# Performance work log

Hardware: AMD Instinct MI355X
Metric: run time of the kernel (lower is better)

The kernel has to match this reference:

```python
import jax, jax.numpy as jnp
import numpy as np

BLOCK = 8
C = 64


def setup_inputs() -> dict:
    key = jax.random.key(0)
    k = jax.random.split(key, 6)
    B, H, W = 4, 512, 512
    x = jax.random.normal(k[0], (B, C, H, W), jnp.float32)
    # per-channel 8x8 transform matrices (torch.randn init)
    tw = jax.random.normal(k[1], (C, BLOCK, BLOCK), jnp.float32)
    s = 1.0 / np.sqrt(C).astype(np.float32)
    w1 = jax.random.normal(k[2], (C, C), jnp.float32) * s  # 1x1 conv weight [out,in]
    b1 = jax.random.normal(k[3], (C,), jnp.float32) * s
    w2 = jax.random.normal(k[4], (C, C), jnp.float32) * s
    b2 = jax.random.normal(k[5], (C,), jnp.float32) * s
    return {"x": x, "tw": tw, "w1": w1, "b1": b1, "w2": w2, "b2": b2}


def reference(x, tw, w1, b1, w2, b2):
    B, Cc, H, W = x.shape
    bs = BLOCK
    nh, nw = H // bs, W // bs
    # extract 8x8 blocks: [b,c,nh,nw,i,j]
    p = x.reshape(B, Cc, nh, bs, nw, bs).transpose(0, 1, 2, 4, 3, 5)
    # per-channel T @ P @ T^T : out[p,q] = T[p,i] P[i,j] T[q,j]
    t = jnp.einsum('cpi,bcnmij,cqj->bcnmpq', tw, p, tw)
    # fold blocks back to image
    y = t.transpose(0, 1, 2, 4, 3, 5).reshape(B, Cc, H, W)
    # quantization gate: 1x1 conv -> relu -> 1x1 conv -> sigmoid
    g = jnp.einsum('oc,bchw->bohw', w1, y) + b1[None, :, None, None]
    g = jax.nn.relu(g)
    g = jnp.einsum('oc,bchw->bohw', w2, g) + b2[None, :, None, None]
    g = jax.nn.sigmoid(g)
    return y * g
```

## Files before the change

kernel.cpp:

```cpp
#include <hip/hip_runtime.h>

typedef float f4 __attribute__((ext_vector_type(4)));
typedef __attribute__((ext_vector_type(4))) float f32x4;
typedef _Float16 h8 __attribute__((ext_vector_type(8)));

__device__ __forceinline__ void gload_lds16(const float* g, float* l) {
    __builtin_amdgcn_global_load_lds(
        (const __attribute__((address_space(1))) void*)g,
        (__attribute__((address_space(3))) void*)l, 16, 0, 0);
}

__global__ __launch_bounds__(256, 2)
void avif_pipe(const float* __restrict__ x, const float* __restrict__ twm,
               const float* __restrict__ w1, const float* __restrict__ b1,
               const float* __restrict__ w2, const float* __restrict__ b2,
               float* __restrict__ out)
{
    __shared__ float xs[8192];
    __shared__ ushort ysf[128][64];
    __shared__ ushort hsf[128][64];

    const int t = threadIdx.x;
    const int bid = blockIdx.x;
    const int wc = bid & 1;
    const int hb = (bid >> 1) & 63;
    const int b  = bid >> 7;

    const int wv = t >> 6, lane = t & 63;
    const int li = lane & 15, lg = lane >> 4, l7 = li & 7;
    const int lb3 = (li >> 3) << 2;

    const float* xslab = x + (((size_t)(b * 64)) * 512 + (size_t)hb * 8) * 512 + wc * 256;
    const float* gp[8];
#pragma unroll
    for (int j = 0; j < 8; ++j) {
        const int G = j * 256 + t;
        const int c = G >> 5;
        const int v = (G & 31) ^ (c & 7);
        const int r = v >> 2, qg = v & 3;
        gp[j] = xslab + (size_t)c * 262144 + r * 512 + qg * 4;
    }
    float* lbase = &xs[wv * 256];

    h8 w1f[2], w2f[2];
    {
        const float* p1 = w1 + (16 * wv + li) * 64 + lg * 8;
        const float* p2 = w2 + (16 * wv + li) * 64 + lg * 8;
#pragma unroll
        for (int kk = 0; kk < 2; ++kk) {
            f4 a = *(const f4*)(p1 + kk * 32);
            f4 d = *(const f4*)(p1 + kk * 32 + 4);
            h8 f;
#pragma unroll
            for (int q = 0; q < 4; ++q) { f[q] = (_Float16)a[q]; f[4 + q] = (_Float16)d[q]; }
            w1f[kk] = f;
            a = *(const f4*)(p2 + kk * 32);
            d = *(const f4*)(p2 + kk * 32 + 4);
#pragma unroll
            for (int q = 0; q < 4; ++q) { f[q] = (_Float16)a[q]; f[4 + q] = (_Float16)d[q]; }
            w2f[kk] = f;
        }
    }
    const int o0 = 16 * wv + 4 * lg;
    const f4 b1v = *(const f4*)(b1 + o0);
    const float b2s = b2[16 * wv + li];
    const int sg0 = ((lg       ^ l7 ^ lb3) << 3);
    const int sg1 = (((4 + lg) ^ l7 ^ lb3) << 3);
    const int go  = o0 >> 3, co = 4 * (lg & 1);
    const int ch  = 16 * wv + li;
    const int cgE = ch >> 3, c7E = li & 7;

    const int pid = t >> 1, h2 = t & 1;
    const int c   = pid & 63, blk = pid >> 6, Q0 = 4 * h2;
    const float* tB = twm + c * 64;
    const int sc = c * 128, swc = c & 7;
    const int cg = c >> 3, c7 = c & 7;

#pragma unroll
    for (int j = 0; j < 8; ++j) gload_lds16(gp[j], lbase + j * 1024);
    asm volatile("s_waitcnt vmcnt(0)" ::: "memory");
    __syncthreads();

    for (int tile = 0; tile < 16; ++tile) {
        const int wt = wc * 16 + tile;

        {
            float M[8][4];
            {
                f4 Ph[8];
#pragma unroll
                for (int i = 0; i < 8; ++i)
                    Ph[i] = *(const f4*)&xs[sc + ((i * 4 + blk * 2) ^ swc) * 4];
#pragma unroll
                for (int qq = 0; qq < 4; ++qq) {
                    f4 Th = *(const f4*)(tB + (Q0 + qq) * 8);
#pragma unroll
                    for (int i = 0; i < 8; ++i) {
                        float s = Ph[i][0] * Th[0];
                        s = fmaf(Ph[i][1], Th[1], s);
                        s = fmaf(Ph[i][2], Th[2], s);
                        s = fmaf(Ph[i][3], Th[3], s);
                        M[i][qq] = s;
                    }
                }
#pragma unroll
                for (int i = 0; i < 8; ++i)
                    Ph[i] = *(const f4*)&xs[sc + ((i * 4 + blk * 2 + 1) ^ swc) * 4];
#pragma unroll
                for (int qq = 0; qq < 4; ++qq) {
                    f4 Th = *(const f4*)(tB + (Q0 + qq) * 8 + 4);
#pragma unroll
                    for (int i = 0; i < 8; ++i) {
                        float s = M[i][qq];
                        s = fmaf(Ph[i][0], Th[0], s);
                        s = fmaf(Ph[i][1], Th[1], s);
                        s = fmaf(Ph[i][2], Th[2], s);
                        s = fmaf(Ph[i][3], Th[3], s);
                        M[i][qq] = s;
                    }
                }
            }
#pragma unroll
            for (int p = 0; p < 8; ++p) {
                f4 a = *(const f4*)(tB + p * 8);
                f4 d = *(const f4*)(tB + p * 8 + 4);
                const int px0 = p * 16 + blk * 8;
#pragma unroll
                for (int qq = 0; qq < 4; ++qq) {
                    const int q = Q0 + qq;
                    float s = a[0] * M[0][qq];
                    s = fmaf(a[1], M[1][qq], s);
                    s = fmaf(a[2], M[2][qq], s);
                    s = fmaf(a[3], M[3][qq], s);
                    s = fmaf(d[0], M[4][qq], s);
                    s = fmaf(d[1], M[5][qq], s);
                    s = fmaf(d[2], M[6][qq], s);
                    s = fmaf(d[3], M[7][qq], s);
                    const int idx = ((cg ^ q ^ (blk << 2)) << 3) | c7;
                    *(_Float16*)&ysf[px0 + q][idx] = (_Float16)s;
                }
            }
        }
        __syncthreads();

        if (tile < 15) {
#pragma unroll
            for (int j = 0; j < 8; ++j)
                gload_lds16(gp[j] + (tile + 1) * 16, lbase + j * 1024);
        }

        f32x4 acc[8];
#pragma unroll
        for (int j = 0; j < 8; ++j) acc[j] = (f32x4){0.f, 0.f, 0.f, 0.f};
#pragma unroll
        for (int j = 0; j < 8; ++j) {
            const int row = 16 * j + li;
            h8 bh0 = *(const h8*)&ysf[row][sg0];
            h8 bh1 = *(const h8*)&ysf[row][sg1];
            acc[j] = __builtin_amdgcn_mfma_f32_16x16x32_f16(w1f[0], bh0, acc[j], 0, 0, 0);
            acc[j] = __builtin_amdgcn_mfma_f32_16x16x32_f16(w1f[1], bh1, acc[j], 0, 0, 0);
        }
#pragma unroll
        for (int j = 0; j < 8; ++j) {
            const int px = 16 * j + li;
            const int idx = ((go ^ l7 ^ lb3) << 3) + co;
            union { _Float16 h[2]; unsigned u; } p01, p23;
            p01.h[0] = (_Float16)fmaxf(acc[j][0] + b1v[0], 0.f);
            p01.h[1] = (_Float16)fmaxf(acc[j][1] + b1v[1], 0.f);
            p23.h[0] = (_Float16)fmaxf(acc[j][2] + b1v[2], 0.f);
            p23.h[1] = (_Float16)fmaxf(acc[j][3] + b1v[3], 0.f);
            *(unsigned*)&hsf[px][idx]     = p01.u;
            *(unsigned*)&hsf[px][idx + 2] = p23.u;
        }
        asm volatile("s_waitcnt vmcnt(0)" ::: "memory");
        __syncthreads();

#pragma unroll
        for (int j = 0; j < 8; ++j) acc[j] = (f32x4){0.f, 0.f, 0.f, 0.f};
#pragma unroll
        for (int j = 0; j < 8; ++j) {
            const int row = 16 * j + li;
            h8 ah0 = *(const h8*)&hsf[row][sg0];
            h8 ah1 = *(const h8*)&hsf[row][sg1];
            acc[j] = __builtin_amdgcn_mfma_f32_16x16x32_f16(ah0, w2f[0], acc[j], 0, 0, 0);
            acc[j] = __builtin_amdgcn_mfma_f32_16x16x32_f16(ah1, w2f[1], acc[j], 0, 0, 0);
        }
        float* oB = out + ((size_t)(b * 64) + ch) * 262144
                    + (size_t)(hb * 8) * 512 + wt * 16 + 4 * lg;
#pragma unroll
        for (int j = 0; j < 8; ++j) {
            f4 r;
#pragma unroll
            for (int r4 = 0; r4 < 4; ++r4) {
                const int pc = 4 * lg + r4;
                const int px = 16 * j + pc;
                const int idx = ((cgE ^ (pc & 7) ^ (((pc >> 3) & 1) << 2)) << 3) | c7E;
                float yv = (float)(*(const _Float16*)&ysf[px][idx]);
                float z = acc[j][r4] + b2s;
                float g = __builtin_amdgcn_rcpf(1.f + __expf(-z));
                r[r4] = yv * g;
            }
            *(f4*)(oB + (size_t)j * 512) = r;
        }
        __syncthreads();
    }
}

extern "C" void kernel_launch(void* const* d_in, const int* in_sizes, int n_in,
                              void* d_out, int out_size, void* d_ws, size_t ws_size,
                              hipStream_t stream) {
    (void)in_sizes; (void)n_in; (void)out_size; (void)d_ws; (void)ws_size;
    const float* x   = (const float*)d_in[0];
    const float* twm = (const float*)d_in[1];
    const float* w1  = (const float*)d_in[2];
    const float* b1  = (const float*)d_in[3];
    const float* w2  = (const float*)d_in[4];
    const float* b2  = (const float*)d_in[5];
    float* out = (float*)d_out;

    avif_pipe<<<dim3(512), dim3(256), 0, stream>>>(x, twm, w1, b1, w2, b2, out);
}
```

Before: 170.2 us.

## Load input blocks directly into registers and split work across more blocks

Drops the LDS staging buffer for the input slab. Each thread now loads its own 8x4 half-block straight into registers and exchanges the other half with its pair via a lane shuffle, prefetching the next tile's registers during compute. The grid grows from 512 to 2048 blocks, each doing 4 interleaved tiles instead of 16, and occupancy is raised to 3 blocks per SM. Barriers become a raw s_barrier with only an lgkmcnt wait. This frees LDS and raises parallelism, at the cost of uncoalesced 16-byte global loads and more register pressure.

```diff
diff --git a/kernel.cpp b/kernel.cpp
--- a/kernel.cpp
+++ b/kernel.cpp
@@ -4,43 +4,29 @@
 typedef __attribute__((ext_vector_type(4))) float f32x4;
 typedef _Float16 h8 __attribute__((ext_vector_type(8)));
 
-__device__ __forceinline__ void gload_lds16(const float* g, float* l) {
-    __builtin_amdgcn_global_load_lds(
-        (const __attribute__((address_space(1))) void*)g,
-        (__attribute__((address_space(3))) void*)l, 16, 0, 0);
-}
-
-__global__ __launch_bounds__(256, 2)
-void avif_pipe(const float* __restrict__ x, const float* __restrict__ twm,
-               const float* __restrict__ w1, const float* __restrict__ b1,
-               const float* __restrict__ w2, const float* __restrict__ b2,
-               float* __restrict__ out)
+#define BAR() do { asm volatile("s_waitcnt lgkmcnt(0)" ::: "memory"); \
+    __builtin_amdgcn_s_barrier(); asm volatile("" ::: "memory"); } while (0)
+
+__global__ __launch_bounds__(256, 3)
+void avif_reg(const float* __restrict__ x, const float* __restrict__ twm,
+              const float* __restrict__ w1, const float* __restrict__ b1,
+              const float* __restrict__ w2, const float* __restrict__ b2,
+              float* __restrict__ out)
 {
-    __shared__ float xs[8192];
     __shared__ ushort ysf[128][64];
     __shared__ ushort hsf[128][64];
 
     const int t = threadIdx.x;
     const int bid = blockIdx.x;
-    const int wc = bid & 1;
-    const int hb = (bid >> 1) & 63;
-    const int b  = bid >> 7;
+    const int wc = (bid >> 3) & 1;
+    const int u  = ((bid >> 4) << 3) | (bid & 7);
+    const int ks = u & 3;
+    const int hb = (u >> 2) & 63;
+    const int b  = u >> 8;
 
     const int wv = t >> 6, lane = t & 63;
     const int li = lane & 15, lg = lane >> 4, l7 = li & 7;
     const int lb3 = (li >> 3) << 2;
-
-    const float* xslab = x + (((size_t)(b * 64)) * 512 + (size_t)hb * 8) * 512 + wc * 256;
-    const float* gp[8];
-#pragma unroll
-    for (int j = 0; j < 8; ++j) {
-        const int G = j * 256 + t;
-        const int c = G >> 5;
-        const int v = (G & 31) ^ (c & 7);
-        const int r = v >> 2, qg = v & 3;
-        gp[j] = xslab + (size_t)c * 262144 + r * 512 + qg * 4;
-    }
-    float* lbase = &xs[wv * 256];
 
     h8 w1f[2], w2f[2];
     {
@@ -73,81 +59,73 @@
     const int pid = t >> 1, h2 = t & 1;
     const int c   = pid & 63, blk = pid >> 6, Q0 = 4 * h2;
     const float* tB = twm + c * 64;
-    const int sc = c * 128, swc = c & 7;
+    const float* xb = x + ((size_t)(b * 64 + c) * 512 + hb * 8) * 512
+                        + blk * 8 + 4 * h2;
     const int cg = c >> 3, c7 = c & 7;
 
-#pragma unroll
-    for (int j = 0; j < 8; ++j) gload_lds16(gp[j], lbase + j * 1024);
-    asm volatile("s_waitcnt vmcnt(0)" ::: "memory");
-    __syncthreads();
-
-    for (int tile = 0; tile < 16; ++tile) {
-        const int wt = wc * 16 + tile;
-
+    int wt = 2 * (ks * 4) + wc;
+
+    f4 Pr[8];
+#pragma unroll
+    for (int i = 0; i < 8; ++i)
+        Pr[i] = *(const f4*)(xb + (size_t)i * 512 + wt * 16);
+
+#pragma unroll 1
+    for (int it = 0; it < 4; ++it) {
+        float M[8][4];
         {
-            float M[8][4];
-            {
-                f4 Ph[8];
-#pragma unroll
-                for (int i = 0; i < 8; ++i)
-                    Ph[i] = *(const f4*)&xs[sc + ((i * 4 + blk * 2) ^ swc) * 4];
+            f4 Tq0[4], Tq1[4];
+#pragma unroll
+            for (int qq = 0; qq < 4; ++qq) {
+                Tq0[qq] = *(const f4*)(tB + (Q0 + qq) * 8 + 4 * h2);
+                Tq1[qq] = *(const f4*)(tB + (Q0 + qq) * 8 + 4 * (1 - h2));
+            }
+#pragma unroll
+            for (int i = 0; i < 8; ++i) {
+                f4 Px;
+#pragma unroll
+                for (int e = 0; e < 4; ++e) Px[e] = __shfl_xor(Pr[i][e], 1);
 #pragma unroll
                 for (int qq = 0; qq < 4; ++qq) {
-                    f4 Th = *(const f4*)(tB + (Q0 + qq) * 8);
-#pragma unroll
-                    for (int i = 0; i < 8; ++i) {
-                        float s = Ph[i][0] * Th[0];
-                        s = fmaf(Ph[i][1], Th[1], s);
-                        s = fmaf(Ph[i][2], Th[2], s);
-                        s = fmaf(Ph[i][3], Th[3], s);
-                        M[i][qq] = s;
-                    }
+                    float s = Pr[i][0] * Tq0[qq][0];
+                    s = fmaf(Pr[i][1], Tq0[qq][1], s);
+                    s = fmaf(Pr[i][2], Tq0[qq][2], s);
+                    s = fmaf(Pr[i][3], Tq0[qq][3], s);
+                    s = fmaf(Px[0], Tq1[qq][0], s);
+                    s = fmaf(Px[1], Tq1[qq][1], s);
+                    s = fmaf(Px[2], Tq1[qq][2], s);
+                    s = fmaf(Px[3], Tq1[qq][3], s);
+                    M[i][qq] = s;
                 }
-#pragma unroll
-                for (int i = 0; i < 8; ++i)
-                    Ph[i] = *(const f4*)&xs[sc + ((i * 4 + blk * 2 + 1) ^ swc) * 4];
-#pragma unroll
-                for (int qq = 0; qq < 4; ++qq) {
-                    f4 Th = *(const f4*)(tB + (Q0 + qq) * 8 + 4);
-#pragma unroll
-                    for (int i = 0; i < 8; ++i) {
-                        float s = M[i][qq];
-                        s = fmaf(Ph[i][0], Th[0], s);
-                        s = fmaf(Ph[i][1], Th[1], s);
-                        s = fmaf(Ph[i][2], Th[2], s);
-                        s = fmaf(Ph[i][3], Th[3], s);
-                        M[i][qq] = s;
-                    }
-                }
-            }
-#pragma unroll
-            for (int p = 0; p < 8; ++p) {
-                f4 a = *(const f4*)(tB + p * 8);
-                f4 d = *(const f4*)(tB + p * 8 + 4);
-                const int px0 = p * 16 + blk * 8;
-#pragma unroll
-                for (int qq = 0; qq < 4; ++qq) {
-                    const int q = Q0 + qq;
-                    float s = a[0] * M[0][qq];
-                    s = fmaf(a[1], M[1][qq], s);
-                    s = fmaf(a[2], M[2][qq], s);
-                    s = fmaf(a[3], M[3][qq], s);
-                    s = fmaf(d[0], M[4][qq], s);
-                    s = fmaf(d[1], M[5][qq], s);
-                    s = fmaf(d[2], M[6][qq], s);
-                    s = fmaf(d[3], M[7][qq], s);
-                    const int idx = ((cg ^ q ^ (blk << 2)) << 3) | c7;
-                    *(_Float16*)&ysf[px0 + q][idx] = (_Float16)s;
-                }
-            }
-        }
-        __syncthreads();
-
-        if (tile < 15) {
-#pragma unroll
-            for (int j = 0; j < 8; ++j)
-                gload_lds16(gp[j] + (tile + 1) * 16, lbase + j * 1024);
-        }
+            }
+        }
+        if (it < 3) {
+            const int wtn = wt + 2;
+#pragma unroll
+            for (int i = 0; i < 8; ++i)
+                Pr[i] = *(const f4*)(xb + (size_t)i * 512 + wtn * 16);
+        }
+#pragma unroll
+        for (int p = 0; p < 8; ++p) {
+            f4 a = *(const f4*)(tB + p * 8);
+            f4 d = *(const f4*)(tB + p * 8 + 4);
+            const int px0 = p * 16 + blk * 8;
+#pragma unroll
+            for (int qq = 0; qq < 4; ++qq) {
+                const int q = Q0 + qq;
+                float s = a[0] * M[0][qq];
+                s = fmaf(a[1], M[1][qq], s);
+                s = fmaf(a[2], M[2][qq], s);
+                s = fmaf(a[3], M[3][qq], s);
+                s = fmaf(d[0], M[4][qq], s);
+                s = fmaf(d[1], M[5][qq], s);
+                s = fmaf(d[2], M[6][qq], s);
+                s = fmaf(d[3], M[7][qq], s);
+                const int idx = ((cg ^ q ^ (blk << 2)) << 3) | c7;
+                *(_Float16*)&ysf[px0 + q][idx] = (_Float16)s;
+            }
+        }
+        BAR();
 
         f32x4 acc[8];
 #pragma unroll
@@ -172,8 +150,7 @@
             *(unsigned*)&hsf[px][idx]     = p01.u;
             *(unsigned*)&hsf[px][idx + 2] = p23.u;
         }
-        asm volatile("s_waitcnt vmcnt(0)" ::: "memory");
-        __syncthreads();
+        BAR();
 
 #pragma unroll
         for (int j = 0; j < 8; ++j) acc[j] = (f32x4){0.f, 0.f, 0.f, 0.f};
@@ -202,7 +179,9 @@
             }
             *(f4*)(oB + (size_t)j * 512) = r;
         }
-        __syncthreads();
+        BAR();
+
+        wt += 2;
     }
 }
 
@@ -218,5 +197,5 @@
     const float* b2  = (const float*)d_in[5];
     float* out = (float*)d_out;
 
-    avif_pipe<<<dim3(512), dim3(256), 0, stream>>>(x, twm, w1, b1, w2, b2, out);
+    avif_reg<<<dim3(2048), dim3(256), 0, stream>>>(x, twm, w1, b1, w2, b2, out);
 }
```

Result: slower. 334.2 us (+96.3%).
